# Optimization experiments

Hardware: AMD Instinct MI355X
Metric: run time of the kernel (lower is better)

Reference implementation:

```python
import math
import jax, jax.numpy as jnp
import numpy as np

B, L, D, H = 2, 2048, 512, 8
HD = D // H
PADDING_IDX = 0


def _sinusoid_table(num_embeddings, dim, padding_idx):
    # matches RelativeSinusoidalPositionalEmbedding.get_embedding
    half = dim // 2
    inv = math.log(10000.0) / (half - 1)
    freqs = jnp.exp(jnp.arange(half, dtype=jnp.float32) * (-inv))
    ang = jnp.arange(num_embeddings, dtype=jnp.float32)[:, None] * freqs[None, :]
    emb = jnp.concatenate([jnp.sin(ang), jnp.cos(ang)], axis=1)  # [N, dim]
    return emb.at[padding_idx].set(0.0)


def _rel_pos_embed(seq_len):
    # RelativeEmbedding.forward: init table size 513 (origin_shift=257); since
    # padding_idx + seq_len > 257 it regenerates with num_embeddings = 2*seq_len,
    # origin_shift = seq_len. All static at trace time.
    init_origin = 512 // 2 + 1
    if PADDING_IDX + seq_len > init_origin:
        num = (PADDING_IDX + seq_len) * 2
        origin = num // 2
    else:
        num = 512 + 1
        origin = init_origin
    table = _sinusoid_table(num, HD, PADDING_IDX)
    positions = jnp.arange(-seq_len, seq_len) + origin  # [2L]
    return table[positions]  # [2L, HD]


def _shift(BD):
    # [B,H,L,2L] -> [B,H,L,L], Transformer-XL relative shift
    b, h, l, _ = BD.shape
    BD = jnp.concatenate([BD, jnp.zeros((b, h, l, 1), BD.dtype)], axis=-1)
    BD = BD.reshape(b, h, -1, l)[:, :, :-1].reshape(b, h, l, -1)
    return BD[:, :, :, l:]


def setup_inputs() -> dict:
    key = jax.random.key(0)
    ks = jax.random.split(key, 7)
    s = 1.0 / math.sqrt(D)
    return {
        "q": jax.random.normal(ks[0], (B, L, D), jnp.float32),
        "k": jax.random.normal(ks[1], (B, L, D), jnp.float32),
        "mask": jnp.ones((B, L, L), jnp.int32),
        "Wq": jax.random.normal(ks[2], (D, D), jnp.float32) * s,
        "Wkv": jax.random.normal(ks[3], (2 * D, D), jnp.float32) * s,
        "Wr": jax.random.normal(ks[4], (HD, HD), jnp.float32) * (1.0 / math.sqrt(HD)),
        "r_r_bias": jax.random.normal(ks[5], (H, HD), jnp.float32) * 0.1,
        "r_w_bias": jax.random.normal(ks[6], (H, HD), jnp.float32) * 0.1,
    }


def reference(q, k, mask, Wq, Wkv, Wr, r_r_bias, r_w_bias):
    b, l, d = q.shape
    scale = math.sqrt(HD)

    pos = _rel_pos_embed(l)                # [2L, HD]
    r = pos @ Wr.T                          # [2L, HD]

    qp = q @ Wq.T                           # [B,L,D]
    kv = k @ Wkv.T                          # [B,L,2D]
    kk, vv = jnp.split(kv, 2, axis=-1)

    qh = qp.reshape(b, l, H, HD).transpose(0, 2, 1, 3)  # [B,H,L,HD]
    kh = kk.reshape(b, l, H, HD).transpose(0, 2, 1, 3)
    vh = vv.reshape(b, l, H, HD).transpose(0, 2, 1, 3)

    rw_head_q = qh + r_r_bias[None, :, None, :]
    AC = jnp.einsum('bnqd,bnkd->bnqk', rw_head_q, kh)        # [B,H,L,L]
    D_ = jnp.einsum('nd,ld->nl', r_w_bias, r)[None, :, None, :]  # [1,H,1,2L]
    B_ = jnp.einsum('bnqd,ld->bnql', qh, r)                  # [B,H,L,2L]
    BD = _shift(B_ + D_)                                      # [B,H,L,L]

    attn = (AC + BD) / scale
    attn = jnp.where(mask[:, None, :, :] == 0, -jnp.inf, attn)
    attn = jax.nn.softmax(attn, axis=-1)

    out = jnp.einsum('bnqk,bnkd->bnqd', attn, vh)
    out = out.transpose(0, 2, 1, 3).reshape(b, l, d)
    return (out, attn)
```

## Files before the change

### kernel.cpp

```cpp
#include <hip/hip_runtime.h>
#include <math.h>

#define NL 2048
#define N2L 4096

typedef __attribute__((ext_vector_type(8))) short bf16x8;
typedef __attribute__((ext_vector_type(4))) float f32x4;
#define MFMA(a,b,c) __builtin_amdgcn_mfma_f32_16x16x32_bf16((a),(b),(c),0,0,0)

#define BARRIER() do {                                        \
    __builtin_amdgcn_sched_barrier(0);                        \
    asm volatile("s_waitcnt lgkmcnt(0)" ::: "memory");        \
    __builtin_amdgcn_s_barrier();                             \
    __builtin_amdgcn_sched_barrier(0);                        \
  } while (0)

__device__ __forceinline__ unsigned short bf16_rne(float x){
  unsigned int u = __float_as_uint(x);
  u += 0x7FFFu + ((u>>16)&1u);
  return (unsigned short)(u>>16);
}
__device__ __forceinline__ float bf16_to_f(unsigned short h){
  return __uint_as_float(((unsigned int)h)<<16);
}

__global__ __launch_bounds__(256) void split_kernel(
    const float* __restrict__ q, const float* __restrict__ k,
    const float* __restrict__ Wq, const float* __restrict__ Wkv,
    unsigned short* __restrict__ qsh, unsigned short* __restrict__ qsl,
    unsigned short* __restrict__ ksh, unsigned short* __restrict__ ksl,
    unsigned short* __restrict__ wqh, unsigned short* __restrict__ wql,
    unsigned short* __restrict__ wkh, unsigned short* __restrict__ wkl) {
  const int C1 = 524288, C2 = 1048576, C3 = 1114112, C4 = 1245184;
  for (int i = blockIdx.x * blockDim.x + threadIdx.x; i < C4; i += gridDim.x * blockDim.x) {
    const float* src; unsigned short *dh, *dl; int j;
    if (i < C1)      { src = q;   dh = qsh; dl = qsl; j = i; }
    else if (i < C2) { src = k;   dh = ksh; dl = ksl; j = i - C1; }
    else if (i < C3) { src = Wq;  dh = wqh; dl = wql; j = i - C2; }
    else             { src = Wkv; dh = wkh; dl = wkl; j = i - C3; }
    float4 v = reinterpret_cast<const float4*>(src)[j];
    unsigned short h0 = bf16_rne(v.x), h1 = bf16_rne(v.y), h2 = bf16_rne(v.z), h3 = bf16_rne(v.w);
    unsigned short l0 = bf16_rne(v.x - bf16_to_f(h0));
    unsigned short l1 = bf16_rne(v.y - bf16_to_f(h1));
    unsigned short l2 = bf16_rne(v.z - bf16_to_f(h2));
    unsigned short l3 = bf16_rne(v.w - bf16_to_f(h3));
    reinterpret_cast<uint2*>(dh)[j] = make_uint2((unsigned)h0 | ((unsigned)h1 << 16),
                                                 (unsigned)h2 | ((unsigned)h3 << 16));
    reinterpret_cast<uint2*>(dl)[j] = make_uint2((unsigned)l0 | ((unsigned)l1 << 16),
                                                 (unsigned)l2 | ((unsigned)l3 << 16));
  }
}

__global__ __launch_bounds__(256) void maskpack_kernel(
    const int* __restrict__ mask, unsigned char* __restrict__ mb) {
  int row = blockIdx.x;
  int t = threadIdx.x;
  const int* mr = mask + (size_t)row * 2048 + t * 8;
  int4 a = *(const int4*)mr;
  int4 c = *(const int4*)(mr + 4);
  unsigned v = (a.x != 0) | ((a.y != 0) << 1) | ((a.z != 0) << 2) | ((a.w != 0) << 3) |
               ((c.x != 0) << 4) | ((c.y != 0) << 5) | ((c.z != 0) << 6) | ((c.w != 0) << 7);
  mb[(size_t)row * 256 + t] = (unsigned char)v;
}

__global__ void build_r_kernel(const float* __restrict__ Wr,
                               const float* __restrict__ rrb,
                               const float* __restrict__ rwb,
                               unsigned short* __restrict__ rh,
                               unsigned short* __restrict__ rl,
                               float* __restrict__ cTab) {
  int n = blockIdx.x;
  int t = threadIdx.x;
  __shared__ float pos[64];
  float v = 0.f;
  if (n != 0) {
    int j = t & 31;
    float inv = logf(10000.f) * (1.0f / 31.0f);
    float freq = expf(-inv * (float)j);
    float ang = (float)n * freq;
    v = (t < 32) ? sinf(ang) : cosf(ang);
  }
  pos[t] = v;
  __syncthreads();
  float acc = 0.f;
  const float* wrow = Wr + t * 64;
  #pragma unroll
  for (int j = 0; j < 64; ++j) acc += pos[j] * wrow[j];
  unsigned short hh = bf16_rne(acc);
  rh[n * 64 + t] = hh;
  rl[n * 64 + t] = bf16_rne(acc - bf16_to_f(hh));
  #pragma unroll
  for (int h = 0; h < 8; ++h) {
    float pr = acc * (rwb[h * 64 + t] - rrb[h * 64 + t]);
    #pragma unroll
    for (int off = 1; off < 64; off <<= 1) pr += __shfl_xor(pr, off);
    if (t == 0) cTab[h * N2L + n] = pr;
  }
}

__global__ __launch_bounds__(256) void proj_kernel(
    const unsigned short* __restrict__ qsh, const unsigned short* __restrict__ qsl,
    const unsigned short* __restrict__ ksh, const unsigned short* __restrict__ ksl,
    const unsigned short* __restrict__ wqh, const unsigned short* __restrict__ wql,
    const unsigned short* __restrict__ wkh, const unsigned short* __restrict__ wkl,
    const float* __restrict__ rrb,
    unsigned short* __restrict__ qAh, unsigned short* __restrict__ qAl,
    unsigned short* __restrict__ khh, unsigned short* __restrict__ khl,
    unsigned short* __restrict__ vTh, unsigned short* __restrict__ vTl) {
  int tid = threadIdx.x;
  int w = tid >> 6, lane = tid & 63, li = lane & 15, g = lane >> 4;
  int bx = blockIdx.x, by = blockIdx.y;
  f32x4 acc[4];
  #pragma unroll
  for (int i = 0; i < 4; ++i) { acc[i][0]=0.f; acc[i][1]=0.f; acc[i][2]=0.f; acc[i][3]=0.f; }

  if (by < 16) {
    int n0 = by * 64, m0 = bx * 64;
    const unsigned short* Xh = (n0 < 512) ? qsh : ksh;
    const unsigned short* Xl = (n0 < 512) ? qsl : ksl;
    const unsigned short* Wh = (n0 < 512) ? (wqh + (size_t)n0 * 512) : (wkh + (size_t)(n0 - 512) * 512);
    const unsigned short* Wl = (n0 < 512) ? (wql + (size_t)n0 * 512) : (wkl + (size_t)(n0 - 512) * 512);
    int rowm = m0 + 16 * w + li;
    for (int ks = 0; ks < 16; ++ks) {
      int d0 = ks * 32 + 8 * g;
      bf16x8 ah = *(const bf16x8*)(Xh + (size_t)rowm * 512 + d0);
      bf16x8 al = *(const bf16x8*)(Xl + (size_t)rowm * 512 + d0);
      #pragma unroll
      for (int nt = 0; nt < 4; ++nt) {
        bf16x8 bh_ = *(const bf16x8*)(Wh + (size_t)(16 * nt + li) * 512 + d0);
        bf16x8 bl_ = *(const bf16x8*)(Wl + (size_t)(16 * nt + li) * 512 + d0);
        acc[nt] = MFMA(ah, bh_, acc[nt]);
        acc[nt] = MFMA(al, bh_, acc[nt]);
        acc[nt] = MFMA(ah, bl_, acc[nt]);
      }
    }
    if (n0 < 512) {
      int h = n0 >> 6;
      #pragma unroll
      for (int nt = 0; nt < 4; ++nt) {
        int d = 16 * nt + li;
        float rrv = rrb[h * 64 + d];
        #pragma unroll
        for (int r = 0; r < 4; ++r) {
          int m = m0 + 16 * w + 4 * g + r;
          int b = m >> 11, lt = m & 2047;
          size_t base = (((size_t)(b * 8 + h)) * 2048 + lt) * 64 + d;
          float a1 = acc[nt][r] + rrv;
          unsigned short h1 = bf16_rne(a1);
          qAh[base] = h1; qAl[base] = bf16_rne(a1 - bf16_to_f(h1));
        }
      }
    } else {
      int h = (n0 - 512) >> 6;
      #pragma unroll
      for (int nt = 0; nt < 4; ++nt) {
        int d = 16 * nt + li;
        #pragma unroll
        for (int r = 0; r < 4; ++r) {
          int m = m0 + 16 * w + 4 * g + r;
          int b = m >> 11, lt = m & 2047;
          size_t base = (((size_t)(b * 8 + h)) * 2048 + lt) * 64 + d;
          unsigned short h1 = bf16_rne(acc[nt][r]);
          khh[base] = h1; khl[base] = bf16_rne(acc[nt][r] - bf16_to_f(h1));
        }
      }
    }
  } else {
    int fy = by - 16, m0 = bx * 64, f0 = fy * 64;
    const unsigned short* Ah = wkh + (size_t)(512 + f0 + 16 * w + li) * 512;
    const unsigned short* Al = wkl + (size_t)(512 + f0 + 16 * w + li) * 512;
    for (int ks = 0; ks < 16; ++ks) {
      int d0 = ks * 32 + 8 * g;
      bf16x8 ah = *(const bf16x8*)(Ah + d0);
      bf16x8 al = *(const bf16x8*)(Al + d0);
      #pragma unroll
      for (int nt = 0; nt < 4; ++nt) {
        bf16x8 bh_ = *(const bf16x8*)(ksh + (size_t)(m0 + 16 * nt + li) * 512 + d0);
        bf16x8 bl_ = *(const bf16x8*)(ksl + (size_t)(m0 + 16 * nt + li) * 512 + d0);
        acc[nt] = MFMA(ah, bh_, acc[nt]);
        acc[nt] = MFMA(al, bh_, acc[nt]);
        acc[nt] = MFMA(ah, bl_, acc[nt]);
      }
    }
    int h = fy;
    #pragma unroll
    for (int nt = 0; nt < 4; ++nt) {
      int m = m0 + 16 * nt + li;
      int b = m >> 11, lt = m & 2047;
      #pragma unroll
      for (int r = 0; r < 4; ++r) {
        int d = 16 * w + 4 * g + r;
        size_t base = (((size_t)(b * 8 + h)) * 64 + d) * 2048 + lt;
        unsigned short h1 = bf16_rne(acc[nt][r]);
        vTh[base] = h1; vTl[base] = bf16_rne(acc[nt][r] - bf16_to_f(h1));
      }
    }
  }
}

__global__ __launch_bounds__(256) void attn_kernel(
    const unsigned short* __restrict__ qAh, const unsigned short* __restrict__ qAl,
    const unsigned short* __restrict__ khh, const unsigned short* __restrict__ khl,
    const unsigned short* __restrict__ vTh, const unsigned short* __restrict__ vTl,
    const unsigned short* __restrict__ rh, const unsigned short* __restrict__ rl,
    const float* __restrict__ cTab, const unsigned char* __restrict__ mb,
    float* __restrict__ attnp, float* __restrict__ oPart, float* __restrict__ rlbuf) {
  __shared__ float Tlds[96 * 34];
  __shared__ unsigned int Plds[2048];
  __shared__ float lw[4][32];

  int tid = threadIdx.x;
  int w = tid >> 6, lane = tid & 63, li = lane & 15, g = lane >> 4;
  int q0 = blockIdx.x * 32;
  int y = blockIdx.y, kh = y & 1, bh = y >> 1, b = bh >> 3, h = bh & 7;
  const unsigned short* qAhp = qAh + (size_t)bh * 131072;
  const unsigned short* qAlp = qAl + (size_t)bh * 131072;
  const unsigned short* khhp = khh + (size_t)bh * 131072;
  const unsigned short* khlp = khl + (size_t)bh * 131072;
  const unsigned short* vThp = vTh + (size_t)bh * 131072;
  const unsigned short* vTlp = vTl + (size_t)bh * 131072;
  const float* cTabh = cTab + (size_t)h * N2L;
  float* attn_bh = attnp + (size_t)bh * NL * NL;

  bf16x8 fAh[2][2], fAl[2][2];
  #pragma unroll
  for (int nt = 0; nt < 2; ++nt)
    #pragma unroll
    for (int ks = 0; ks < 2; ++ks) {
      size_t o = (size_t)(q0 + 16 * nt + li) * 64 + 32 * ks + 8 * g;
      fAh[nt][ks] = *(const bf16x8*)(qAhp + o);
      fAl[nt][ks] = *(const bf16x8*)(qAlp + o);
    }

  float lrun[2] = {0.f, 0.f};
  f32x4 accO[2];
  #pragma unroll
  for (int i = 0; i < 2; ++i) { accO[i][0]=0.f; accO[i][1]=0.f; accO[i][2]=0.f; accO[i][3]=0.f; }

  int kt0 = kh * 16, ktEnd = kt0 + 16;
  int mcol = 2 * w + (g >> 1);
  int mshift = (g & 1) * 4;

  for (int kt = kt0; kt < ktEnd; ++kt) {
    int k0 = kt * 64;
    int nlo = k0 - q0 + 2016;
    unsigned int mbyte[2];
    #pragma unroll
    for (int nt = 0; nt < 2; ++nt)
      mbyte[nt] = mb[((size_t)b * NL + q0 + 16 * nt + li) * 256 + (k0 >> 3) + mcol];
    bf16x8 vhf[2], vlf[2];
    #pragma unroll
    for (int ks = 0; ks < 2; ++ks) {
      size_t vo = (size_t)(16 * w + li) * NL + k0 + 32 * ks + 8 * g;
      vhf[ks] = *(const bf16x8*)(vThp + vo);
      vlf[ks] = *(const bf16x8*)(vTlp + vo);
    }
    float4 cvs[3];
    #pragma unroll
    for (int pp = 0; pp < 3; ++pp) {
      int pi = w * 3 + pp, jt = pi >> 1;
      cvs[pp] = *(const float4*)(cTabh + nlo + jt * 16 + 4 * g);
    }
    int krow = k0 + 16 * w + li;
    f32x4 accS[2];
    #pragma unroll
    for (int i = 0; i < 2; ++i) { accS[i][0]=0.f; accS[i][1]=0.f; accS[i][2]=0.f; accS[i][3]=0.f; }
    __builtin_amdgcn_s_setprio(1);
    #pragma unroll
    for (int ks = 0; ks < 2; ++ks) {
      size_t o = (size_t)krow * 64 + 32 * ks + 8 * g;
      bf16x8 ah = *(const bf16x8*)(khhp + o);
      bf16x8 al = *(const bf16x8*)(khlp + o);
      #pragma unroll
      for (int nt = 0; nt < 2; ++nt) {
        accS[nt] = MFMA(ah, fAh[nt][ks], accS[nt]);
        accS[nt] = MFMA(al, fAh[nt][ks], accS[nt]);
        accS[nt] = MFMA(ah, fAl[nt][ks], accS[nt]);
      }
    }
    f32x4 accT[3];
    #pragma unroll
    for (int i = 0; i < 3; ++i) { accT[i][0]=0.f; accT[i][1]=0.f; accT[i][2]=0.f; accT[i][3]=0.f; }
    #pragma unroll
    for (int pp = 0; pp < 3; ++pp) {
      int pi = w * 3 + pp, jt = pi >> 1, ntp = pi & 1;
      int rrow = nlo + jt * 16 + li;
      #pragma unroll
      for (int ks = 0; ks < 2; ++ks) {
        size_t o = (size_t)rrow * 64 + 32 * ks + 8 * g;
        bf16x8 ah = *(const bf16x8*)(rh + o);
        bf16x8 al = *(const bf16x8*)(rl + o);
        accT[pp] = MFMA(ah, fAh[ntp][ks], accT[pp]);
        accT[pp] = MFMA(al, fAh[ntp][ks], accT[pp]);
        accT[pp] = MFMA(ah, fAl[ntp][ks], accT[pp]);
      }
    }
    __builtin_amdgcn_s_setprio(0);
    #pragma unroll
    for (int pp = 0; pp < 3; ++pp) {
      int pi = w * 3 + pp, jt = pi >> 1, ntp = pi & 1;
      const float* cv = (const float*)&cvs[pp];
      #pragma unroll
      for (int r = 0; r < 4; ++r)
        Tlds[(jt * 16 + 4 * g + r) * 34 + ntp * 16 + li] = accT[pp][r] + cv[r];
    }
    BARRIER();
    #pragma unroll
    for (int nt = 0; nt < 2; ++nt) {
      int ql_ = 16 * nt + li;
      int qg = q0 + ql_;
      float p[4];
      #pragma unroll
      for (int r = 0; r < 4; ++r) {
        int kl = 16 * w + 4 * g + r;
        float sv = (accS[nt][r] + Tlds[(kl - ql_ + 32) * 34 + ql_]) * 0.125f;
        p[r] = ((mbyte[nt] >> (mshift + r)) & 1u) ? __expf(sv) : 0.f;
      }
      *(float4*)(attn_bh + (size_t)qg * NL + k0 + 16 * w + 4 * g) =
          make_float4(p[0], p[1], p[2], p[3]);
      lrun[nt] += p[0] + p[1] + p[2] + p[3];
      unsigned short h0 = bf16_rne(p[0]), h1 = bf16_rne(p[1]);
      unsigned short h2 = bf16_rne(p[2]), h3 = bf16_rne(p[3]);
      unsigned short e0 = bf16_rne(p[0] - bf16_to_f(h0)), e1 = bf16_rne(p[1] - bf16_to_f(h1));
      unsigned short e2 = bf16_rne(p[2] - bf16_to_f(h2)), e3 = bf16_rne(p[3] - bf16_to_f(h3));
      unsigned int poff = (unsigned)(ql_ * 128 + (((16 * w + 4 * g) * 2) ^ ((ql_ & 7) << 4)));
      *(uint2*)((char*)Plds + poff) =
          make_uint2((unsigned)h0 | ((unsigned)h1 << 16), (unsigned)h2 | ((unsigned)h3 << 16));
      *(uint2*)((char*)Plds + 4096 + poff) =
          make_uint2((unsigned)e0 | ((unsigned)e1 << 16), (unsigned)e2 | ((unsigned)e3 << 16));
    }
    BARRIER();
    __builtin_amdgcn_s_setprio(1);
    #pragma unroll
    for (int ks = 0; ks < 2; ++ks) {
      #pragma unroll
      for (int nt = 0; nt < 2; ++nt) {
        unsigned int ro = (unsigned)((16 * nt + li) * 128 + (((32 * ks + 8 * g) * 2) ^ ((li & 7) << 4)));
        bf16x8 ph = *(const bf16x8*)((const char*)Plds + ro);
        bf16x8 pl = *(const bf16x8*)((const char*)Plds + 4096 + ro);
        accO[nt] = MFMA(vhf[ks], ph, accO[nt]);
        accO[nt] = MFMA(vlf[ks], ph, accO[nt]);
        accO[nt] = MFMA(vhf[ks], pl, accO[nt]);
      }
    }
    __builtin_amdgcn_s_setprio(0);
    BARRIER();
  }

  #pragma unroll
  for (int nt = 0; nt < 2; ++nt) {
    lrun[nt] += __shfl_xor(lrun[nt], 16);
    lrun[nt] += __shfl_xor(lrun[nt], 32);
  }
  if (lane < 16) { lw[w][li] = lrun[0]; lw[w][16 + li] = lrun[1]; }
  BARRIER();
  if (tid < 32)
    rlbuf[(size_t)kh * 32768 + (size_t)bh * 2048 + q0 + tid] =
        lw[0][tid] + lw[1][tid] + lw[2][tid] + lw[3][tid];
  float* op = oPart + (size_t)kh * 2097152 + (size_t)bh * 131072;
  #pragma unroll
  for (int nt = 0; nt < 2; ++nt) {
    int qg = q0 + 16 * nt + li;
    int d = 16 * w + 4 * g;
    *(float4*)(op + (size_t)qg * 64 + d) =
        make_float4(accO[nt][0], accO[nt][1], accO[nt][2], accO[nt][3]);
  }
}

__global__ __launch_bounds__(256) void combine_kernel(
    const float* __restrict__ oPart, const float* __restrict__ rlbuf,
    float* __restrict__ outp) {
  int bh = blockIdx.y, b = bh >> 3, h = bh & 7;
  int q = blockIdx.x * 4 + (threadIdx.x >> 6);
  int d = threadIdx.x & 63;
  size_t i0 = ((size_t)bh * 2048 + q) * 64 + d;
  float l = rlbuf[(size_t)bh * 2048 + q] + rlbuf[32768 + (size_t)bh * 2048 + q];
  float o = oPart[i0] + oPart[2097152 + i0];
  outp[((size_t)b * 2048 + q) * 512 + h * 64 + d] = o / l;
}

__global__ __launch_bounds__(256) void rescale_kernel(
    const float* __restrict__ rlbuf, float* __restrict__ attnp) {
  int row = blockIdx.x;
  int bh = blockIdx.y;
  float rv = 1.0f / (rlbuf[(size_t)bh * 2048 + row] + rlbuf[32768 + (size_t)bh * 2048 + row]);
  float* ap = attnp + ((size_t)bh * NL + row) * NL + threadIdx.x * 8;
  float4 a = *(float4*)ap;
  float4 b2 = *(float4*)(ap + 4);
  *(float4*)ap = make_float4(a.x * rv, a.y * rv, a.z * rv, a.w * rv);
  *(float4*)(ap + 4) = make_float4(b2.x * rv, b2.y * rv, b2.z * rv, b2.w * rv);
}

extern "C" void kernel_launch(void* const* d_in, const int* in_sizes, int n_in,
                              void* d_out, int out_size, void* d_ws, size_t ws_size,
                              hipStream_t stream) {
  const float* q    = (const float*)d_in[0];
  const float* k    = (const float*)d_in[1];
  const int*   mask = (const int*)d_in[2];
  const float* Wq   = (const float*)d_in[3];
  const float* Wkv  = (const float*)d_in[4];
  const float* Wr   = (const float*)d_in[5];
  const float* rrb  = (const float*)d_in[6];
  const float* rwb  = (const float*)d_in[7];

  float* outp  = (float*)d_out;
  float* attnp = outp + (size_t)2 * NL * 512;

  unsigned short* W = (unsigned short*)d_ws;
  const size_t RHI = 0,            RLO = RHI + 262144;
  const size_t QSH = RLO + 262144, QSL = QSH + 2097152;
  const size_t KSH = QSL + 2097152, KSL = KSH + 2097152;
  const size_t WQH = KSL + 2097152, WQL = WQH + 262144;
  const size_t WKH = WQL + 262144,  WKL = WKH + 524288;
  const size_t QAH = WKL + 524288,  QAL = QAH + 2097152;
  const size_t KHH = QAL + 2097152, KHL = KHH + 2097152;
  const size_t VTH = KHL + 2097152, VTL = VTH + 2097152;
  const size_t RLB = VTL + 2097152;
  const size_t CTB = RLB + 131072;
  const size_t MBB = CTB + 65536;
  float* rlbuf = (float*)(W + RLB);
  float* cTab  = (float*)(W + CTB);
  unsigned char* mb = (unsigned char*)(W + MBB);
  float* oPart = (float*)(W + QSH);

  hipLaunchKernelGGL(split_kernel, dim3(1024), dim3(256), 0, stream,
                     q, k, Wq, Wkv, W+QSH, W+QSL, W+KSH, W+KSL, W+WQH, W+WQL, W+WKH, W+WKL);
  hipLaunchKernelGGL(maskpack_kernel, dim3(4096), dim3(256), 0, stream, mask, mb);
  hipLaunchKernelGGL(build_r_kernel, dim3(N2L), dim3(64), 0, stream,
                     Wr, rrb, rwb, W+RHI, W+RLO, cTab);
  hipLaunchKernelGGL(proj_kernel, dim3(64, 24), dim3(256), 0, stream,
                     W+QSH, W+QSL, W+KSH, W+KSL, W+WQH, W+WQL, W+WKH, W+WKL, rrb,
                     W+QAH, W+QAL, W+KHH, W+KHL, W+VTH, W+VTL);
  hipLaunchKernelGGL(attn_kernel, dim3(64, 32), dim3(256), 0, stream,
                     W+QAH, W+QAL, W+KHH, W+KHL, W+VTH, W+VTL,
                     W+RHI, W+RLO, cTab, mb, attnp, oPart, rlbuf);
  hipLaunchKernelGGL(combine_kernel, dim3(512, 16), dim3(256), 0, stream,
                     oPart, rlbuf, outp);
  hipLaunchKernelGGL(rescale_kernel, dim3(NL, 16), dim3(256), 0, stream,
                     rlbuf, attnp);
}
```

Before: 600.1 us.

## Split attention key loop across two wave groups per block

Doubles the attention block to 512 threads with two groups of four waves, each processing alternating 64-key tiles with its own LDS buffers. The two groups' partial output accumulators and row sums are merged through shared memory at the end. This targets per-block latency by putting more waves in flight on the serialized key loop. The cost is more LDS and register pressure per block and block-wide barriers that now synchronise both groups, which may reduce the number of resident blocks.

```diff
diff --git a/kernel.cpp b/kernel.cpp
--- a/kernel.cpp
+++ b/kernel.cpp
@@ -198,19 +198,22 @@
   }
 }
 
-__global__ __launch_bounds__(256) void attn_kernel(
+__global__ __launch_bounds__(512) void attn_kernel(
     const unsigned short* __restrict__ qAh, const unsigned short* __restrict__ qAl,
     const unsigned short* __restrict__ khh, const unsigned short* __restrict__ khl,
     const unsigned short* __restrict__ vTh, const unsigned short* __restrict__ vTl,
     const unsigned short* __restrict__ rh, const unsigned short* __restrict__ rl,
     const float* __restrict__ cTab, const unsigned char* __restrict__ mb,
     float* __restrict__ attnp, float* __restrict__ oPart, float* __restrict__ rlbuf) {
-  __shared__ float Tlds[96 * 34];
-  __shared__ unsigned int Plds[2048];
-  __shared__ float lw[4][32];
+  __shared__ float Tlds[2][96 * 34];
+  __shared__ unsigned int Plds[2][2048];
+  __shared__ float lw[8][32];
 
   int tid = threadIdx.x;
-  int w = tid >> 6, lane = tid & 63, li = lane & 15, g = lane >> 4;
+  int w8 = tid >> 6;
+  int grp = w8 >> 2;
+  int w = w8 & 3;
+  int lane = tid & 63, li = lane & 15, g = lane >> 4;
   int q0 = blockIdx.x * 32;
   int y = blockIdx.y, kh = y & 1, bh = y >> 1, b = bh >> 3, h = bh & 7;
   const unsigned short* qAhp = qAh + (size_t)bh * 131072;
@@ -221,6 +224,8 @@
   const unsigned short* vTlp = vTl + (size_t)bh * 131072;
   const float* cTabh = cTab + (size_t)h * N2L;
   float* attn_bh = attnp + (size_t)bh * NL * NL;
+  float* Tg = Tlds[grp];
+  unsigned int* Pg = Plds[grp];
 
   bf16x8 fAh[2][2], fAl[2][2];
   #pragma unroll
@@ -237,11 +242,12 @@
   #pragma unroll
   for (int i = 0; i < 2; ++i) { accO[i][0]=0.f; accO[i][1]=0.f; accO[i][2]=0.f; accO[i][3]=0.f; }
 
-  int kt0 = kh * 16, ktEnd = kt0 + 16;
+  int kt0 = kh * 16;
   int mcol = 2 * w + (g >> 1);
   int mshift = (g & 1) * 4;
 
-  for (int kt = kt0; kt < ktEnd; ++kt) {
+  for (int it = 0; it < 8; ++it) {
+    int kt = kt0 + 2 * it + grp;
     int k0 = kt * 64;
     int nlo = k0 - q0 + 2016;
     unsigned int mbyte[2];
@@ -302,7 +308,7 @@
       const float* cv = (const float*)&cvs[pp];
       #pragma unroll
       for (int r = 0; r < 4; ++r)
-        Tlds[(jt * 16 + 4 * g + r) * 34 + ntp * 16 + li] = accT[pp][r] + cv[r];
+        Tg[(jt * 16 + 4 * g + r) * 34 + ntp * 16 + li] = accT[pp][r] + cv[r];
     }
     BARRIER();
     #pragma unroll
@@ -313,7 +319,7 @@
       #pragma unroll
       for (int r = 0; r < 4; ++r) {
         int kl = 16 * w + 4 * g + r;
-        float sv = (accS[nt][r] + Tlds[(kl - ql_ + 32) * 34 + ql_]) * 0.125f;
+        float sv = (accS[nt][r] + Tg[(kl - ql_ + 32) * 34 + ql_]) * 0.125f;
         p[r] = ((mbyte[nt] >> (mshift + r)) & 1u) ? __expf(sv) : 0.f;
       }
       *(float4*)(attn_bh + (size_t)qg * NL + k0 + 16 * w + 4 * g) =
@@ -324,9 +330,9 @@
       unsigned short e0 = bf16_rne(p[0] - bf16_to_f(h0)), e1 = bf16_rne(p[1] - bf16_to_f(h1));
       unsigned short e2 = bf16_rne(p[2] - bf16_to_f(h2)), e3 = bf16_rne(p[3] - bf16_to_f(h3));
       unsigned int poff = (unsigned)(ql_ * 128 + (((16 * w + 4 * g) * 2) ^ ((ql_ & 7) << 4)));
-      *(uint2*)((char*)Plds + poff) =
+      *(uint2*)((char*)Pg + poff) =
           make_uint2((unsigned)h0 | ((unsigned)h1 << 16), (unsigned)h2 | ((unsigned)h3 << 16));
-      *(uint2*)((char*)Plds + 4096 + poff) =
+      *(uint2*)((char*)Pg + 4096 + poff) =
           make_uint2((unsigned)e0 | ((unsigned)e1 << 16), (unsigned)e2 | ((unsigned)e3 << 16));
     }
     BARRIER();
@@ -336,8 +342,8 @@
       #pragma unroll
       for (int nt = 0; nt < 2; ++nt) {
         unsigned int ro = (unsigned)((16 * nt + li) * 128 + (((32 * ks + 8 * g) * 2) ^ ((li & 7) << 4)));
-        bf16x8 ph = *(const bf16x8*)((const char*)Plds + ro);
-        bf16x8 pl = *(const bf16x8*)((const char*)Plds + 4096 + ro);
+        bf16x8 ph = *(const bf16x8*)((const char*)Pg + ro);
+        bf16x8 pl = *(const bf16x8*)((const char*)Pg + 4096 + ro);
         accO[nt] = MFMA(vhf[ks], ph, accO[nt]);
         accO[nt] = MFMA(vlf[ks], ph, accO[nt]);
         accO[nt] = MFMA(vhf[ks], pl, accO[nt]);
@@ -352,18 +358,31 @@
     lrun[nt] += __shfl_xor(lrun[nt], 16);
     lrun[nt] += __shfl_xor(lrun[nt], 32);
   }
-  if (lane < 16) { lw[w][li] = lrun[0]; lw[w][16 + li] = lrun[1]; }
+  if (lane < 16) { lw[w8][li] = lrun[0]; lw[w8][16 + li] = lrun[1]; }
+  float* Oac = Tlds[0];
+  if (grp == 1) {
+    #pragma unroll
+    for (int nt = 0; nt < 2; ++nt)
+      #pragma unroll
+      for (int r = 0; r < 4; ++r)
+        Oac[(16 * nt + li) * 64 + 16 * w + 4 * g + r] = accO[nt][r];
+  }
   BARRIER();
   if (tid < 32)
     rlbuf[(size_t)kh * 32768 + (size_t)bh * 2048 + q0 + tid] =
-        lw[0][tid] + lw[1][tid] + lw[2][tid] + lw[3][tid];
-  float* op = oPart + (size_t)kh * 2097152 + (size_t)bh * 131072;
-  #pragma unroll
-  for (int nt = 0; nt < 2; ++nt) {
-    int qg = q0 + 16 * nt + li;
-    int d = 16 * w + 4 * g;
-    *(float4*)(op + (size_t)qg * 64 + d) =
-        make_float4(accO[nt][0], accO[nt][1], accO[nt][2], accO[nt][3]);
+        lw[0][tid] + lw[1][tid] + lw[2][tid] + lw[3][tid] +
+        lw[4][tid] + lw[5][tid] + lw[6][tid] + lw[7][tid];
+  if (grp == 0) {
+    float* op = oPart + (size_t)kh * 2097152 + (size_t)bh * 131072;
+    #pragma unroll
+    for (int nt = 0; nt < 2; ++nt) {
+      int qg = q0 + 16 * nt + li;
+      int d = 16 * w + 4 * g;
+      const float* oa = &Oac[(16 * nt + li) * 64 + d];
+      *(float4*)(op + (size_t)qg * 64 + d) =
+          make_float4(accO[nt][0] + oa[0], accO[nt][1] + oa[1],
+                      accO[nt][2] + oa[2], accO[nt][3] + oa[3]);
+    }
   }
 }
 
@@ -431,7 +450,7 @@
   hipLaunchKernelGGL(proj_kernel, dim3(64, 24), dim3(256), 0, stream,
                      W+QSH, W+QSL, W+KSH, W+KSL, W+WQH, W+WQL, W+WKH, W+WKL, rrb,
                      W+QAH, W+QAL, W+KHH, W+KHL, W+VTH, W+VTL);
-  hipLaunchKernelGGL(attn_kernel, dim3(64, 32), dim3(256), 0, stream,
+  hipLaunchKernelGGL(attn_kernel, dim3(64, 32), dim3(512), 0, stream,
                      W+QAH, W+QAL, W+KHH, W+KHL, W+VTH, W+VTL,
                      W+RHI, W+RLO, cTab, mb, attnp, oPart, rlbuf);
   hipLaunchKernelGGL(combine_kernel, dim3(512, 16), dim3(256), 0, stream,
```

Result: slower. 729.7 us (+21.6%).
